# Performance work log

Hardware: AMD Instinct MI355X
Metric: run time of the kernel (lower is better)

## Reference

```python
import jax, jax.numpy as jnp
import numpy as np
import math

NUM_HEADS = 12
HEAD_DIM = 64
DEGREE = 3
POLY_DIM = HEAD_DIM * (DEGREE + 1)  # 256
MEM_HID = 512
HIDDEN = 768


def setup_inputs() -> dict:
    key = jax.random.key(0)
    ks = jax.random.split(key, 6)
    B, S = 4, 2048
    hidden_states = jax.random.normal(ks[0], (B, S, HIDDEN), dtype=jnp.float32)
    # q projection weight stored (in, out) so y = x @ Wq
    Wq = jax.random.normal(ks[1], (HIDDEN, HIDDEN), dtype=jnp.float32) / np.sqrt(HIDDEN)
    # polynomial coefficients initialized to 1/i!
    coeffs = jnp.array([1.0 / math.factorial(i) for i in range(DEGREE + 1)], dtype=jnp.float32)
    # deep memory MLP: Linear(poly_dim->mem_hid) + ReLU + Linear(mem_hid->poly_dim)
    W1 = jax.random.normal(ks[2], (POLY_DIM, MEM_HID), dtype=jnp.float32) / np.sqrt(POLY_DIM)
    b1 = jnp.zeros((MEM_HID,), dtype=jnp.float32)
    W2 = jax.random.normal(ks[3], (MEM_HID, POLY_DIM), dtype=jnp.float32) / np.sqrt(MEM_HID)
    b2 = jnp.zeros((POLY_DIM,), dtype=jnp.float32)
    return {"hidden_states": hidden_states, "Wq": Wq, "coeffs": coeffs,
            "W1": W1, "b1": b1, "W2": W2, "b2": b2}


def _poly_map(x, coeffs):
    # x: [..., head_dim] -> [..., head_dim*(degree+1)]
    xs = jnp.clip(x, -10.0, 10.0)
    feats = [coeffs[0] * jnp.ones_like(x)]
    for i in range(1, DEGREE + 1):
        feats.append(jnp.clip(coeffs[i] * xs ** i, -1e6, 1e6))
    return jnp.concatenate(feats, axis=-1)


def reference(hidden_states, Wq, coeffs, W1, b1, W2, b2):
    B, S, H = hidden_states.shape
    # q projection -> [B, S, nh, hd]
    q = (hidden_states @ Wq).reshape(B, S, NUM_HEADS, HEAD_DIM)
    # polynomial feature expansion -> [B, S, nh, poly_dim]
    poly_q = _poly_map(q, coeffs)
    flat = poly_q.reshape(-1, POLY_DIM)  # [B*S*nh, poly_dim]
    # deep memory MLP (test-time memory read)
    h = jax.nn.relu(flat @ W1 + b1)
    mem = h @ W2 + b2  # [B*S*nh, poly_dim]
    # slice first head_dim dims, fold heads back into hidden
    out = mem[:, :HEAD_DIM].reshape(B, S, NUM_HEADS * HEAD_DIM)
    return out
```

## Files before the change

kernel.cpp:

```cpp
#include <hip/hip_runtime.h>


typedef unsigned short u16;
typedef __attribute__((ext_vector_type(8))) short short8;
typedef __attribute__((ext_vector_type(4))) float f32x4;
typedef __attribute__((ext_vector_type(4))) u16 u16x4;

__device__ __forceinline__ u16 f2bf(float f) {
    unsigned u = __builtin_bit_cast(unsigned, f);
    u += 0x7FFFu + ((u >> 16) & 1u);
    return (u16)(u >> 16);
}

__device__ __forceinline__ void gl2lds16(const void* g, void* l) {
    __builtin_amdgcn_global_load_lds(
        (const __attribute__((address_space(1))) unsigned int*)g,
        (__attribute__((address_space(3))) unsigned int*)l, 16, 0, 0);
}


__global__ __launch_bounds__(256) void cast_f32_bf16(const float* __restrict__ in,
                                                     u16* __restrict__ out, int n4) {
    int i = blockIdx.x * 256 + threadIdx.x;
    if (i < n4) {
        float4 v = reinterpret_cast<const float4*>(in)[i];
        u16x4 o = {f2bf(v.x), f2bf(v.y), f2bf(v.z), f2bf(v.w)};
        reinterpret_cast<u16x4*>(out)[i] = o;
    }
}

__global__ __launch_bounds__(256) void transpose_cast(const float* __restrict__ in,
                                                      u16* __restrict__ out,
                                                      int R, int Cin) {
    __shared__ float t[32][33];
    const int c0 = blockIdx.x * 32, r0 = blockIdx.y * 32;
    const int tx = threadIdx.x, ty = threadIdx.y;
    #pragma unroll
    for (int j = 0; j < 32; j += 8)
        t[ty + j][tx] = in[(size_t)(r0 + ty + j) * Cin + c0 + tx];
    __syncthreads();
    #pragma unroll
    for (int j = 0; j < 32; j += 8)
        out[(size_t)(c0 + ty + j) * R + r0 + tx] = f2bf(t[tx][ty + j]);
}


template<int BM, int BN, int WTM, int WTN, int K, int LDA, int LDB, int LDC,
         bool POLY, bool RELU, bool BIAS, bool OUTBF>
__global__ __launch_bounds__(256)
void mfma_gemm(const u16* __restrict__ A, const u16* __restrict__ B,
               const float* __restrict__ bias, const float* __restrict__ coeffs,
               void* __restrict__ Cv, const float* __restrict__ Aq)
{
    constexpr int MT = WTM / 16, NT = WTN / 16, GM = BM / WTM;
    __shared__ u16 As[BM * 32];
    __shared__ u16 Bs[BN * 32];

    const int tid = threadIdx.x;
    const int w = tid >> 6, lane = tid & 63;
    const int lrow = lane >> 2, lslot = lane & 3;
    const int m16 = lane & 15, quad = lane >> 4;
    const int bm = blockIdx.x * BM, bn = blockIdx.y * BN;
    const int wr = (w % GM) * WTM, wc = (w / GM) * WTN;

    float c0 = 0.f, c1 = 0.f, c2 = 0.f, c3 = 0.f;
    if constexpr (POLY) { c0 = coeffs[0]; c1 = coeffs[1]; c2 = coeffs[2]; c3 = coeffs[3]; }

    f32x4 acc[MT][NT];
    #pragma unroll
    for (int i = 0; i < MT; ++i)
        #pragma unroll
        for (int j = 0; j < NT; ++j)
            acc[i][j] = (f32x4){0.f, 0.f, 0.f, 0.f};

    for (int k0 = 0; k0 < K; k0 += 32) {
        #pragma unroll
        for (int i = 0; i < BN / 64; ++i) {
            const int row = (w * (BN / 64) + i) * 16 + lrow;
            const int c = lslot ^ ((row >> 2) & 3);
            gl2lds16(B + (size_t)(bn + row) * LDB + k0 + c * 8,
                     &Bs[row * 32 + lslot * 8]);
        }
        #pragma unroll
        for (int i = 0; i < BM / 64; ++i) {
            const int row = (w * (BM / 64) + i) * 16 + lrow;
            const int c = lslot ^ ((row >> 2) & 3);
            if constexpr (POLY) {
                const int oct = k0 >> 6, d0 = k0 & 63;
                const float* qp = Aq + (size_t)(bm + row) * LDA + d0 + c * 8;
                const float4 v0 = *reinterpret_cast<const float4*>(qp);
                const float4 v1 = *reinterpret_cast<const float4*>(qp + 4);
                const float xs[8] = {v0.x, v0.y, v0.z, v0.w, v1.x, v1.y, v1.z, v1.w};
                const float coef = (oct == 0) ? c0 : (oct == 1) ? c1 : (oct == 2) ? c2 : c3;
                short8 sv;
                #pragma unroll
                for (int j = 0; j < 8; ++j) {
                    float p;
                    if (oct == 0) {
                        p = c0;
                    } else {
                        const float x = fminf(fmaxf(xs[j], -10.f), 10.f);
                        float t = x;
                        if (oct >= 2) t *= x;
                        if (oct == 3) t *= x;
                        p = fminf(fmaxf(coef * t, -1e6f), 1e6f);
                    }
                    sv[j] = (short)f2bf(p);
                }
                *reinterpret_cast<short8*>(&As[row * 32 + lslot * 8]) = sv;
            } else {
                gl2lds16(A + (size_t)(bm + row) * LDA + k0 + c * 8,
                         &As[row * 32 + lslot * 8]);
            }
        }
        __syncthreads();

        short8 af[MT], bf[NT];
        #pragma unroll
        for (int i = 0; i < MT; ++i) {
            const int row = wr + i * 16 + m16;
            const int s = quad ^ ((row >> 2) & 3);
            af[i] = *reinterpret_cast<const short8*>(&As[row * 32 + s * 8]);
        }
        #pragma unroll
        for (int j = 0; j < NT; ++j) {
            const int row = wc + j * 16 + m16;
            const int s = quad ^ ((row >> 2) & 3);
            bf[j] = *reinterpret_cast<const short8*>(&Bs[row * 32 + s * 8]);
        }
        #pragma unroll
        for (int i = 0; i < MT; ++i)
            #pragma unroll
            for (int j = 0; j < NT; ++j)
                acc[i][j] = __builtin_amdgcn_mfma_f32_16x16x32_bf16(
                    af[i], bf[j], acc[i][j], 0, 0, 0);
        __syncthreads();
    }

    #pragma unroll
    for (int j = 0; j < NT; ++j) {
        const int col = bn + wc + j * 16 + m16;
        float bv = 0.f;
        if constexpr (BIAS) bv = bias[col];
        #pragma unroll
        for (int i = 0; i < MT; ++i) {
            #pragma unroll
            for (int r = 0; r < 4; ++r) {
                const int row = bm + wr + i * 16 + quad * 4 + r;
                float v = acc[i][j][r] + bv;
                if constexpr (RELU) v = fmaxf(v, 0.f);
                if constexpr (OUTBF)
                    ((u16*)Cv)[(size_t)row * LDC + col] = f2bf(v);
                else
                    ((float*)Cv)[(size_t)row * LDC + col] = v;
            }
        }
    }
}


extern "C" void kernel_launch(void* const* d_in, const int* in_sizes, int n_in,
                              void* d_out, int out_size, void* d_ws, size_t ws_size,
                              hipStream_t stream) {
    const float* X      = (const float*)d_in[0];
    const float* Wq     = (const float*)d_in[1];
    const float* coeffs = (const float*)d_in[2];
    const float* W1     = (const float*)d_in[3];
    const float* b1     = (const float*)d_in[4];
    const float* W2     = (const float*)d_in[5];
    const float* b2     = (const float*)d_in[6];
    float* out = (float*)d_out;

    char* ws = (char*)d_ws;
    u16* Xb  = (u16*)(ws);
    u16* Wqb = (u16*)(ws + 12582912);
    u16* W1b = (u16*)(ws + 13762560);
    u16* W2b = (u16*)(ws + 14024704);
    u16* Hb  = (u16*)(ws + 14090240);
    const size_t reserved = 14090240;

    cast_f32_bf16<<<6144, 256, 0, stream>>>(X, Xb, 8192 * 768 / 4);
    transpose_cast<<<dim3(24, 24), dim3(32, 8), 0, stream>>>(Wq, Wqb, 768, 768);
    transpose_cast<<<dim3(16, 8),  dim3(32, 8), 0, stream>>>(W1, W1b, 256, 512);
    transpose_cast<<<dim3(2, 16),  dim3(32, 8), 0, stream>>>(W2, W2b, 512, 256);

    mfma_gemm<128, 128, 64, 64, 768, 768, 768, 768, false, false, false, false>
        <<<dim3(64, 6), 256, 0, stream>>>(Xb, Wqb, nullptr, nullptr, out, nullptr);

    const long ROWS = 98304;
    long ch = (long)((ws_size > reserved ? ws_size - reserved : 0) / 1024);
    ch &= ~127L;
    if (ch > ROWS) ch = ROWS;
    if (ch < 128) ch = 128;

    for (long r0 = 0; r0 < ROWS; r0 += ch) {
        const long rows = (ROWS - r0 < ch) ? (ROWS - r0) : ch;
        mfma_gemm<128, 128, 64, 64, 256, 64, 256, 512, true, true, true, true>
            <<<dim3(rows / 128, 4), 256, 0, stream>>>(
                nullptr, W1b, b1, coeffs, Hb, out + r0 * 64);
        mfma_gemm<128, 64, 32, 64, 512, 512, 512, 64, false, false, true, false>
            <<<dim3(rows / 128, 1), 256, 0, stream>>>(
                Hb, W2b, b2, nullptr, out + r0 * 64, nullptr);
    }
}
```

Baseline: 185.4 us.

## Fuse poly map, both MLP GEMMs and bias/ReLU into one kernel keeping H in LDS

Replaces the chunked pair of GEMM launches, which wrote and re-read a large bf16 hidden buffer through global memory, with a single fused_mlp kernel. Each block of 64 rows builds the polynomial features in LDS, computes the first GEMM in two halves of 256 hidden units, writes the ReLU output to LDS, and accumulates the second GEMM directly. The hidden-activation round trip to HBM and the extra launches go away. In exchange, weights are read straight from global memory without LDS staging, and the kernel reads q from and writes out into the same buffer. This is safe only because each block reads its own 64 rows before it writes them.

```diff
diff --git a/kernel.cpp b/kernel.cpp
--- a/kernel.cpp
+++ b/kernel.cpp
@@ -45,12 +45,10 @@
 }
 
 
-template<int BM, int BN, int WTM, int WTN, int K, int LDA, int LDB, int LDC,
-         bool POLY, bool RELU, bool BIAS, bool OUTBF>
+template<int BM, int BN, int WTM, int WTN, int K, int LDA, int LDB, int LDC>
 __global__ __launch_bounds__(256)
 void mfma_gemm(const u16* __restrict__ A, const u16* __restrict__ B,
-               const float* __restrict__ bias, const float* __restrict__ coeffs,
-               void* __restrict__ Cv, const float* __restrict__ Aq)
+               float* __restrict__ C)
 {
     constexpr int MT = WTM / 16, NT = WTN / 16, GM = BM / WTM;
     __shared__ u16 As[BM * 32];
@@ -63,9 +61,6 @@
     const int bm = blockIdx.x * BM, bn = blockIdx.y * BN;
     const int wr = (w % GM) * WTM, wc = (w / GM) * WTN;
 
-    float c0 = 0.f, c1 = 0.f, c2 = 0.f, c3 = 0.f;
-    if constexpr (POLY) { c0 = coeffs[0]; c1 = coeffs[1]; c2 = coeffs[2]; c3 = coeffs[3]; }
-
     f32x4 acc[MT][NT];
     #pragma unroll
     for (int i = 0; i < MT; ++i)
@@ -85,33 +80,8 @@
         for (int i = 0; i < BM / 64; ++i) {
             const int row = (w * (BM / 64) + i) * 16 + lrow;
             const int c = lslot ^ ((row >> 2) & 3);
-            if constexpr (POLY) {
-                const int oct = k0 >> 6, d0 = k0 & 63;
-                const float* qp = Aq + (size_t)(bm + row) * LDA + d0 + c * 8;
-                const float4 v0 = *reinterpret_cast<const float4*>(qp);
-                const float4 v1 = *reinterpret_cast<const float4*>(qp + 4);
-                const float xs[8] = {v0.x, v0.y, v0.z, v0.w, v1.x, v1.y, v1.z, v1.w};
-                const float coef = (oct == 0) ? c0 : (oct == 1) ? c1 : (oct == 2) ? c2 : c3;
-                short8 sv;
-                #pragma unroll
-                for (int j = 0; j < 8; ++j) {
-                    float p;
-                    if (oct == 0) {
-                        p = c0;
-                    } else {
-                        const float x = fminf(fmaxf(xs[j], -10.f), 10.f);
-                        float t = x;
-                        if (oct >= 2) t *= x;
-                        if (oct == 3) t *= x;
-                        p = fminf(fmaxf(coef * t, -1e6f), 1e6f);
-                    }
-                    sv[j] = (short)f2bf(p);
-                }
-                *reinterpret_cast<short8*>(&As[row * 32 + lslot * 8]) = sv;
-            } else {
-                gl2lds16(A + (size_t)(bm + row) * LDA + k0 + c * 8,
-                         &As[row * 32 + lslot * 8]);
-            }
+            gl2lds16(A + (size_t)(bm + row) * LDA + k0 + c * 8,
+                     &As[row * 32 + lslot * 8]);
         }
         __syncthreads();
 
@@ -140,20 +110,154 @@
     #pragma unroll
     for (int j = 0; j < NT; ++j) {
         const int col = bn + wc + j * 16 + m16;
-        float bv = 0.f;
-        if constexpr (BIAS) bv = bias[col];
-        #pragma unroll
-        for (int i = 0; i < MT; ++i) {
+        #pragma unroll
+        for (int i = 0; i < MT; ++i)
             #pragma unroll
             for (int r = 0; r < 4; ++r) {
                 const int row = bm + wr + i * 16 + quad * 4 + r;
-                float v = acc[i][j][r] + bv;
-                if constexpr (RELU) v = fmaxf(v, 0.f);
-                if constexpr (OUTBF)
-                    ((u16*)Cv)[(size_t)row * LDC + col] = f2bf(v);
-                else
-                    ((float*)Cv)[(size_t)row * LDC + col] = v;
-            }
+                C[(size_t)row * LDC + col] = acc[i][j][r];
+            }
+    }
+}
+
+
+__global__ __launch_bounds__(256, 2)
+void fused_mlp(const float* __restrict__ q,
+               const u16* __restrict__ W1t,
+               const float* __restrict__ b1,
+               const u16* __restrict__ W2t,
+               const float* __restrict__ b2,
+               const float* __restrict__ coeffs,
+               float* __restrict__ out)
+{
+    __shared__ u16 As[64 * 256];
+    __shared__ u16 Hs[64 * 256];
+
+    const int tid = threadIdx.x;
+    const int w = tid >> 6, lane = tid & 63;
+    const int m16 = lane & 15, quad = lane >> 4;
+    const long bm = (long)blockIdx.x * 64;
+
+    const float c0 = coeffs[0], c1 = coeffs[1], c2 = coeffs[2], c3 = coeffs[3];
+
+    {
+        const int r = tid >> 2;
+        const int ci = tid & 3;
+        const float* qrow = q + (bm + r) * 64;
+        #pragma unroll
+        for (int s = 0; s < 8; ++s) {
+            const int c = ci + 4 * s;
+            const int k0 = c * 8;
+            const int oct = k0 >> 6;
+            const int d0 = k0 & 63;
+            const float4 v0 = *reinterpret_cast<const float4*>(qrow + d0);
+            const float4 v1 = *reinterpret_cast<const float4*>(qrow + d0 + 4);
+            const float xs[8] = {v0.x, v0.y, v0.z, v0.w, v1.x, v1.y, v1.z, v1.w};
+            const float coef = (oct == 0) ? c0 : (oct == 1) ? c1 : (oct == 2) ? c2 : c3;
+            short8 sv;
+            #pragma unroll
+            for (int j = 0; j < 8; ++j) {
+                float p;
+                if (oct == 0) {
+                    p = c0;
+                } else {
+                    const float x = fminf(fmaxf(xs[j], -10.f), 10.f);
+                    float t = x;
+                    if (oct >= 2) t *= x;
+                    if (oct == 3) t *= x;
+                    p = fminf(fmaxf(coef * t, -1e6f), 1e6f);
+                }
+                sv[j] = (short)f2bf(p);
+            }
+            const int slot = c ^ (r & 7);
+            *reinterpret_cast<short8*>(&As[r * 256 + slot * 8]) = sv;
+        }
+    }
+    __syncthreads();
+
+    f32x4 acc2[4];
+    #pragma unroll
+    for (int j = 0; j < 4; ++j) acc2[j] = (f32x4){0.f, 0.f, 0.f, 0.f};
+
+    #pragma unroll 1
+    for (int h = 0; h < 2; ++h) {
+        f32x4 acc1[4][4];
+        #pragma unroll
+        for (int i = 0; i < 4; ++i)
+            #pragma unroll
+            for (int j = 0; j < 4; ++j)
+                acc1[i][j] = (f32x4){0.f, 0.f, 0.f, 0.f};
+
+        #pragma unroll 1
+        for (int ks = 0; ks < 8; ++ks) {
+            const int k0 = ks * 32;
+            short8 af[4], bf[4];
+            #pragma unroll
+            for (int i = 0; i < 4; ++i) {
+                const int row = i * 16 + m16;
+                const int slot = ((k0 >> 3) + quad) ^ (row & 7);
+                af[i] = *reinterpret_cast<const short8*>(&As[row * 256 + slot * 8]);
+            }
+            #pragma unroll
+            for (int j = 0; j < 4; ++j) {
+                const int n = h * 256 + w * 64 + j * 16 + m16;
+                bf[j] = *reinterpret_cast<const short8*>(
+                    &W1t[(size_t)n * 256 + k0 + quad * 8]);
+            }
+            #pragma unroll
+            for (int i = 0; i < 4; ++i)
+                #pragma unroll
+                for (int j = 0; j < 4; ++j)
+                    acc1[i][j] = __builtin_amdgcn_mfma_f32_16x16x32_bf16(
+                        af[i], bf[j], acc1[i][j], 0, 0, 0);
+        }
+
+        #pragma unroll
+        for (int j = 0; j < 4; ++j) {
+            const int nl = w * 64 + j * 16 + m16;
+            const float bv = b1[h * 256 + nl];
+            #pragma unroll
+            for (int i = 0; i < 4; ++i) {
+                #pragma unroll
+                for (int r = 0; r < 4; ++r) {
+                    const int row = i * 16 + quad * 4 + r;
+                    const int slot = (nl >> 3) ^ (row & 7);
+                    const float v = fmaxf(acc1[i][j][r] + bv, 0.f);
+                    Hs[row * 256 + slot * 8 + (nl & 7)] = f2bf(v);
+                }
+            }
+        }
+        __syncthreads();
+
+        #pragma unroll 1
+        for (int ks = 0; ks < 8; ++ks) {
+            const int k0 = ks * 32;
+            short8 hf;
+            {
+                const int row = w * 16 + m16;
+                const int slot = ((k0 >> 3) + quad) ^ (row & 7);
+                hf = *reinterpret_cast<const short8*>(&Hs[row * 256 + slot * 8]);
+            }
+            #pragma unroll
+            for (int j = 0; j < 4; ++j) {
+                const int n = j * 16 + m16;
+                const short8 bf = *reinterpret_cast<const short8*>(
+                    &W2t[(size_t)n * 512 + h * 256 + k0 + quad * 8]);
+                acc2[j] = __builtin_amdgcn_mfma_f32_16x16x32_bf16(
+                    hf, bf, acc2[j], 0, 0, 0);
+            }
+        }
+        __syncthreads();
+    }
+
+    #pragma unroll
+    for (int j = 0; j < 4; ++j) {
+        const int col = j * 16 + m16;
+        const float bv = b2[col];
+        #pragma unroll
+        for (int r = 0; r < 4; ++r) {
+            const long row = bm + w * 16 + quad * 4 + r;
+            out[row * 64 + col] = acc2[j][r] + bv;
         }
     }
 }
@@ -176,30 +280,14 @@
     u16* Wqb = (u16*)(ws + 12582912);
     u16* W1b = (u16*)(ws + 13762560);
     u16* W2b = (u16*)(ws + 14024704);
-    u16* Hb  = (u16*)(ws + 14090240);
-    const size_t reserved = 14090240;
 
     cast_f32_bf16<<<6144, 256, 0, stream>>>(X, Xb, 8192 * 768 / 4);
     transpose_cast<<<dim3(24, 24), dim3(32, 8), 0, stream>>>(Wq, Wqb, 768, 768);
     transpose_cast<<<dim3(16, 8),  dim3(32, 8), 0, stream>>>(W1, W1b, 256, 512);
     transpose_cast<<<dim3(2, 16),  dim3(32, 8), 0, stream>>>(W2, W2b, 512, 256);
 
-    mfma_gemm<128, 128, 64, 64, 768, 768, 768, 768, false, false, false, false>
-        <<<dim3(64, 6), 256, 0, stream>>>(Xb, Wqb, nullptr, nullptr, out, nullptr);
-
-    const long ROWS = 98304;
-    long ch = (long)((ws_size > reserved ? ws_size - reserved : 0) / 1024);
-    ch &= ~127L;
-    if (ch > ROWS) ch = ROWS;
-    if (ch < 128) ch = 128;
-
-    for (long r0 = 0; r0 < ROWS; r0 += ch) {
-        const long rows = (ROWS - r0 < ch) ? (ROWS - r0) : ch;
-        mfma_gemm<128, 128, 64, 64, 256, 64, 256, 512, true, true, true, true>
-            <<<dim3(rows / 128, 4), 256, 0, stream>>>(
-                nullptr, W1b, b1, coeffs, Hb, out + r0 * 64);
-        mfma_gemm<128, 64, 32, 64, 512, 512, 512, 64, false, false, true, false>
-            <<<dim3(rows / 128, 1), 256, 0, stream>>>(
-                Hb, W2b, b2, nullptr, out + r0 * 64, nullptr);
-    }
-}
+    mfma_gemm<128, 128, 64, 64, 768, 768, 768, 768>
+        <<<dim3(64, 6), 256, 0, stream>>>(Xb, Wqb, out);
+
+    fused_mlp<<<1536, 256, 0, stream>>>(out, W1b, b1, W2b, b2, coeffs, out);
+}
```

Result: slower. 217.8 us (+17.5%).

## Shrink GEMM tiles to 64x64, store Q as bf16, cap chunk size

Applied to the files above, without the earlier changes.

All three GEMMs now use a fixed 64x64 block tile with 32x32 warp tiles, and occupancy is hinted via launch bounds (256, 5). The Q projection writes bf16 into a workspace buffer instead of fp32 into the output, so the poly-feature GEMM reads half the bytes for Q. The chunk cap is halved so the memory MLP runs in at least two passes. This launches more, smaller blocks for better occupancy and load balance, at the cost of less data reuse per block and an extra bf16 rounding of Q before the polynomial expansion.

```diff
diff --git a/kernel.cpp b/kernel.cpp
--- a/kernel.cpp
+++ b/kernel.cpp
@@ -3,6 +3,7 @@
 
 typedef unsigned short u16;
 typedef __attribute__((ext_vector_type(8))) short short8;
+typedef __attribute__((ext_vector_type(8))) u16 u16x8;
 typedef __attribute__((ext_vector_type(4))) float f32x4;
 typedef __attribute__((ext_vector_type(4))) u16 u16x4;
 
@@ -10,6 +11,9 @@
     unsigned u = __builtin_bit_cast(unsigned, f);
     u += 0x7FFFu + ((u >> 16) & 1u);
     return (u16)(u >> 16);
+}
+__device__ __forceinline__ float bf2f(u16 h) {
+    return __builtin_bit_cast(float, (unsigned)h << 16);
 }
 
 __device__ __forceinline__ void gl2lds16(const void* g, void* l) {
@@ -45,14 +49,13 @@
 }
 
 
-template<int BM, int BN, int WTM, int WTN, int K, int LDA, int LDB, int LDC,
+template<int BM, int BN, int K, int LDA, int LDB, int LDC,
          bool POLY, bool RELU, bool BIAS, bool OUTBF>
-__global__ __launch_bounds__(256)
+__global__ __launch_bounds__(256, 5)
 void mfma_gemm(const u16* __restrict__ A, const u16* __restrict__ B,
                const float* __restrict__ bias, const float* __restrict__ coeffs,
-               void* __restrict__ Cv, const float* __restrict__ Aq)
+               void* __restrict__ Cv)
 {
-    constexpr int MT = WTM / 16, NT = WTN / 16, GM = BM / WTM;
     __shared__ u16 As[BM * 32];
     __shared__ u16 Bs[BN * 32];
 
@@ -61,89 +64,80 @@
     const int lrow = lane >> 2, lslot = lane & 3;
     const int m16 = lane & 15, quad = lane >> 4;
     const int bm = blockIdx.x * BM, bn = blockIdx.y * BN;
-    const int wr = (w % GM) * WTM, wc = (w / GM) * WTN;
+    const int wr = (w & 1) * 32, wc = (w >> 1) * 32;
 
     float c0 = 0.f, c1 = 0.f, c2 = 0.f, c3 = 0.f;
     if constexpr (POLY) { c0 = coeffs[0]; c1 = coeffs[1]; c2 = coeffs[2]; c3 = coeffs[3]; }
 
-    f32x4 acc[MT][NT];
-    #pragma unroll
-    for (int i = 0; i < MT; ++i)
-        #pragma unroll
-        for (int j = 0; j < NT; ++j)
+    f32x4 acc[2][2];
+    #pragma unroll
+    for (int i = 0; i < 2; ++i)
+        #pragma unroll
+        for (int j = 0; j < 2; ++j)
             acc[i][j] = (f32x4){0.f, 0.f, 0.f, 0.f};
 
     for (int k0 = 0; k0 < K; k0 += 32) {
-        #pragma unroll
-        for (int i = 0; i < BN / 64; ++i) {
-            const int row = (w * (BN / 64) + i) * 16 + lrow;
-            const int c = lslot ^ ((row >> 2) & 3);
-            gl2lds16(B + (size_t)(bn + row) * LDB + k0 + c * 8,
-                     &Bs[row * 32 + lslot * 8]);
-        }
-        #pragma unroll
-        for (int i = 0; i < BM / 64; ++i) {
-            const int row = (w * (BM / 64) + i) * 16 + lrow;
-            const int c = lslot ^ ((row >> 2) & 3);
-            if constexpr (POLY) {
-                const int oct = k0 >> 6, d0 = k0 & 63;
-                const float* qp = Aq + (size_t)(bm + row) * LDA + d0 + c * 8;
-                const float4 v0 = *reinterpret_cast<const float4*>(qp);
-                const float4 v1 = *reinterpret_cast<const float4*>(qp + 4);
-                const float xs[8] = {v0.x, v0.y, v0.z, v0.w, v1.x, v1.y, v1.z, v1.w};
-                const float coef = (oct == 0) ? c0 : (oct == 1) ? c1 : (oct == 2) ? c2 : c3;
-                short8 sv;
-                #pragma unroll
-                for (int j = 0; j < 8; ++j) {
-                    float p;
-                    if (oct == 0) {
-                        p = c0;
-                    } else {
-                        const float x = fminf(fmaxf(xs[j], -10.f), 10.f);
-                        float t = x;
-                        if (oct >= 2) t *= x;
-                        if (oct == 3) t *= x;
-                        p = fminf(fmaxf(coef * t, -1e6f), 1e6f);
-                    }
-                    sv[j] = (short)f2bf(p);
+        const int row = w * 16 + lrow;
+        const int c = lslot ^ ((row >> 2) & 3);
+        gl2lds16(B + (size_t)(bn + row) * LDB + k0 + c * 8,
+                 &Bs[row * 32 + lslot * 8]);
+        if constexpr (POLY) {
+            const int oct = k0 >> 6;
+            const int d0 = (k0 & 63) + c * 8;
+            const u16x8 qv = *reinterpret_cast<const u16x8*>(
+                A + (size_t)(bm + row) * LDA + d0);
+            const float coef = (oct == 0) ? c0 : (oct == 1) ? c1 : (oct == 2) ? c2 : c3;
+            short8 sv;
+            #pragma unroll
+            for (int j = 0; j < 8; ++j) {
+                float p;
+                if (oct == 0) {
+                    p = c0;
+                } else {
+                    const float x = fminf(fmaxf(bf2f(qv[j]), -10.f), 10.f);
+                    float t = x;
+                    if (oct >= 2) t *= x;
+                    if (oct == 3) t *= x;
+                    p = fminf(fmaxf(coef * t, -1e6f), 1e6f);
                 }
-                *reinterpret_cast<short8*>(&As[row * 32 + lslot * 8]) = sv;
-            } else {
-                gl2lds16(A + (size_t)(bm + row) * LDA + k0 + c * 8,
-                         &As[row * 32 + lslot * 8]);
+                sv[j] = (short)f2bf(p);
             }
+            *reinterpret_cast<short8*>(&As[row * 32 + lslot * 8]) = sv;
+        } else {
+            gl2lds16(A + (size_t)(bm + row) * LDA + k0 + c * 8,
+                     &As[row * 32 + lslot * 8]);
         }
         __syncthreads();
 
-        short8 af[MT], bf[NT];
-        #pragma unroll
-        for (int i = 0; i < MT; ++i) {
-            const int row = wr + i * 16 + m16;
-            const int s = quad ^ ((row >> 2) & 3);
-            af[i] = *reinterpret_cast<const short8*>(&As[row * 32 + s * 8]);
-        }
-        #pragma unroll
-        for (int j = 0; j < NT; ++j) {
-            const int row = wc + j * 16 + m16;
-            const int s = quad ^ ((row >> 2) & 3);
-            bf[j] = *reinterpret_cast<const short8*>(&Bs[row * 32 + s * 8]);
-        }
-        #pragma unroll
-        for (int i = 0; i < MT; ++i)
+        short8 af[2], bfr[2];
+        #pragma unroll
+        for (int i = 0; i < 2; ++i) {
+            const int r = wr + i * 16 + m16;
+            const int s = quad ^ ((r >> 2) & 3);
+            af[i] = *reinterpret_cast<const short8*>(&As[r * 32 + s * 8]);
+        }
+        #pragma unroll
+        for (int j = 0; j < 2; ++j) {
+            const int r = wc + j * 16 + m16;
+            const int s = quad ^ ((r >> 2) & 3);
+            bfr[j] = *reinterpret_cast<const short8*>(&Bs[r * 32 + s * 8]);
+        }
+        #pragma unroll
+        for (int i = 0; i < 2; ++i)
             #pragma unroll
-            for (int j = 0; j < NT; ++j)
+            for (int j = 0; j < 2; ++j)
                 acc[i][j] = __builtin_amdgcn_mfma_f32_16x16x32_bf16(
-                    af[i], bf[j], acc[i][j], 0, 0, 0);
+                    af[i], bfr[j], acc[i][j], 0, 0, 0);
         __syncthreads();
     }
 
     #pragma unroll
-    for (int j = 0; j < NT; ++j) {
+    for (int j = 0; j < 2; ++j) {
         const int col = bn + wc + j * 16 + m16;
         float bv = 0.f;
         if constexpr (BIAS) bv = bias[col];
         #pragma unroll
-        for (int i = 0; i < MT; ++i) {
+        for (int i = 0; i < 2; ++i) {
             #pragma unroll
             for (int r = 0; r < 4; ++r) {
                 const int row = bm + wr + i * 16 + quad * 4 + r;
@@ -176,30 +170,31 @@
     u16* Wqb = (u16*)(ws + 12582912);
     u16* W1b = (u16*)(ws + 13762560);
     u16* W2b = (u16*)(ws + 14024704);
-    u16* Hb  = (u16*)(ws + 14090240);
-    const size_t reserved = 14090240;
+    u16* Qb  = (u16*)(ws + 14090240);
+    u16* Hb  = (u16*)(ws + 26673152);
+    const size_t reserved = 26673152;
 
     cast_f32_bf16<<<6144, 256, 0, stream>>>(X, Xb, 8192 * 768 / 4);
     transpose_cast<<<dim3(24, 24), dim3(32, 8), 0, stream>>>(Wq, Wqb, 768, 768);
     transpose_cast<<<dim3(16, 8),  dim3(32, 8), 0, stream>>>(W1, W1b, 256, 512);
     transpose_cast<<<dim3(2, 16),  dim3(32, 8), 0, stream>>>(W2, W2b, 512, 256);
 
-    mfma_gemm<128, 128, 64, 64, 768, 768, 768, 768, false, false, false, false>
-        <<<dim3(64, 6), 256, 0, stream>>>(Xb, Wqb, nullptr, nullptr, out, nullptr);
+    mfma_gemm<64, 64, 768, 768, 768, 768, false, false, false, true>
+        <<<dim3(128, 12), 256, 0, stream>>>(Xb, Wqb, nullptr, nullptr, Qb);
 
     const long ROWS = 98304;
     long ch = (long)((ws_size > reserved ? ws_size - reserved : 0) / 1024);
-    ch &= ~127L;
-    if (ch > ROWS) ch = ROWS;
-    if (ch < 128) ch = 128;
+    ch &= ~63L;
+    if (ch > 49152) ch = 49152;
+    if (ch < 64) ch = 64;
 
     for (long r0 = 0; r0 < ROWS; r0 += ch) {
         const long rows = (ROWS - r0 < ch) ? (ROWS - r0) : ch;
-        mfma_gemm<128, 128, 64, 64, 256, 64, 256, 512, true, true, true, true>
-            <<<dim3(rows / 128, 4), 256, 0, stream>>>(
-                nullptr, W1b, b1, coeffs, Hb, out + r0 * 64);
-        mfma_gemm<128, 64, 32, 64, 512, 512, 512, 64, false, false, true, false>
-            <<<dim3(rows / 128, 1), 256, 0, stream>>>(
-                Hb, W2b, b2, nullptr, out + r0 * 64, nullptr);
-    }
-}
+        mfma_gemm<64, 64, 256, 64, 256, 512, true, true, true, true>
+            <<<dim3(rows / 64, 8), 256, 0, stream>>>(
+                Qb + r0 * 64, W1b, b1, coeffs, Hb);
+        mfma_gemm<64, 64, 512, 512, 512, 64, false, false, true, false>
+            <<<dim3(rows / 64, 1), 256, 0, stream>>>(
+                Hb, W2b, b2, nullptr, out + r0 * 64);
+    }
+}
```

Result: slower. 200.5 us (+8.1%).
